# Kernel optimization log

Hardware: AMD Instinct MI355X
Metric: run time of the kernel (lower is better)

Reference implementation:

```python
import jax, jax.numpy as jnp
import numpy as np

DIM = 1024; HEADS = 8; DHEAD = 64; INNER = HEADS * DHEAD
WS = 512; B = 2; N = 2048; FF = 4 * DIM
NEG = -1e9


def layernorm(x, g, b, eps=1e-5):
    mu = jnp.mean(x, -1, keepdims=True)
    var = jnp.mean((x - mu) ** 2, -1, keepdims=True)
    return (x - mu) * jax.lax.rsqrt(var + eps) * g + b


def rmsnorm(x, g, eps=1e-6):
    return x * jax.lax.rsqrt(jnp.mean(x * x, -1, keepdims=True) + eps) * g


def rotate_half(x):
    x1, x2 = jnp.split(x, 2, -1)
    return jnp.concatenate([-x2, x1], -1)


def local_attention(q, k, v):
    # lucidrains LocalAttention: single-head over last dim, rotary pos emb,
    # window_size=WS, causal, look_backward=1, look_forward=0. n % WS == 0 so autopad no-op.
    b, n, d = q.shape
    w = n // WS
    inv_freq = 1.0 / (10000.0 ** (jnp.arange(0, d, 2, dtype=jnp.float32) / d))
    t = jnp.arange(n)
    freqs = t[:, None].astype(jnp.float32) * inv_freq[None, :]
    emb = jnp.concatenate([freqs, freqs], -1)           # [n, d]
    cos, sin = jnp.cos(emb), jnp.sin(emb)
    q = q * cos + rotate_half(q) * sin
    k = k * cos + rotate_half(k) * sin
    bq = q.reshape(b, w, WS, d) * (d ** -0.5)
    bk = k.reshape(b, w, WS, d)
    bv = v.reshape(b, w, WS, d)

    def look_around(x, pad_value):
        # gather current window + 1 window backward along the window axis
        pads = [(0, 0), (1, 0)] + [(0, 0)] * (x.ndim - 2)
        xp = jnp.pad(x, pads, constant_values=pad_value)
        return jnp.concatenate([xp[:, 0:w], xp[:, 1:w + 1]], axis=2)

    bk = look_around(bk, 0.0)                 # [b, w, 2*WS, d]
    bv = look_around(bv, 0.0)
    bt = t.reshape(w, WS)                     # query positions per window
    bqk = look_around(bt[None], -1)[0]        # key positions, pad = -1  [w, 2*WS]
    sim = jnp.einsum('bwie,bwje->bwij', bq, bk)  # [b, w, WS, 2*WS]
    mask = (bt[:, :, None] < bqk[:, None, :]) | (bqk[:, None, :] == -1)
    sim = jnp.where(mask[None], NEG, sim)
    attn = jax.nn.softmax(sim, -1)
    out = jnp.einsum('bwij,bwje->bwie', attn, bv)
    return out.reshape(b, n, d)


def setup_inputs() -> dict:
    key = jax.random.key(0)
    ks = jax.random.split(key, 10)
    s = 0.02
    f32 = jnp.float32
    return {
        'text': jax.random.normal(ks[0], (B, N, DIM), f32),
        'audio': jax.random.normal(ks[1], (B, N, DIM), f32),
        'video': jax.random.normal(ks[2], (B, N, DIM), f32),
        'Wa': jax.random.normal(ks[3], (DIM, DIM), f32) * s,
        'ba': jnp.zeros((DIM,), f32),
        'lna_g': jnp.ones((DIM,), f32), 'lna_b': jnp.zeros((DIM,), f32),
        'Wvid': jax.random.normal(ks[4], (DIM, DIM), f32) * s,
        'bvid': jnp.zeros((DIM,), f32),
        'lnv_g': jnp.ones((DIM,), f32), 'lnv_b': jnp.zeros((DIM,), f32),
        'ln1_g': jnp.ones((DIM,), f32), 'ln1_b': jnp.zeros((DIM,), f32),
        'Wq': jax.random.normal(ks[5], (DIM, INNER), f32) * s,
        'Wkv': jax.random.normal(ks[6], (DIM, 2 * INNER), f32) * s,
        'qn_g': jnp.ones((DHEAD,), f32), 'kn_g': jnp.ones((DHEAD,), f32),
        'Wo': jax.random.normal(ks[7], (INNER, DIM), f32) * s,
        'W1': jax.random.normal(ks[8], (DIM, FF), f32) * s,
        'b1': jnp.zeros((FF,), f32),
        'ln2_g': jnp.ones((FF,), f32), 'ln2_b': jnp.zeros((FF,), f32),
        'W2': jax.random.normal(ks[9], (FF, DIM), f32) * s,
        'b2': jnp.zeros((DIM,), f32),
    }


def reference(text, audio, video, Wa, ba, lna_g, lna_b, Wvid, bvid, lnv_g, lnv_b,
              ln1_g, ln1_b, Wq, Wkv, qn_g, kn_g, Wo, W1, b1, ln2_g, ln2_b, W2, b2):
    # modality -> text-token adapters (audio_to_text / video_to_text): linear + layernorm
    audio_t = layernorm(audio @ Wa + ba, lna_g, lna_b)
    video_t = layernorm(video @ Wvid + bvid, lnv_g, lnv_b)
    # windowed local attention: q=text, k=audio tokens, v=video tokens
    x = local_attention(text, audio_t, video_t)          # [B, N, DIM]
    # qk-norm full causal attention (flash=False: dense [B,H,N,N] scores)
    b, n, _ = x.shape
    h = layernorm(x, ln1_g, ln1_b)
    q = (h @ Wq).reshape(b, n, HEADS, DHEAD).transpose(0, 2, 1, 3)
    k, v = jnp.split(h @ Wkv, 2, -1)
    k = k.reshape(b, n, HEADS, DHEAD).transpose(0, 2, 1, 3)
    v = v.reshape(b, n, HEADS, DHEAD).transpose(0, 2, 1, 3)
    q = rmsnorm(q, qn_g)
    k = rmsnorm(k, kn_g)
    sim = jnp.einsum('bhid,bhjd->bhij', q, k) * (DHEAD ** -0.5)
    causal = jnp.tril(jnp.ones((n, n), bool))
    sim = jnp.where(causal[None, None], sim, NEG)
    attn = jax.nn.softmax(sim, -1)
    o = jnp.einsum('bhij,bhjd->bhid', attn, v).transpose(0, 2, 1, 3).reshape(b, n, INNER)
    x = o @ Wo
    x = x + x                                            # x = x + x in source
    # FFN: Linear -> GELU -> post-act LayerNorm -> Linear, + residual
    h1 = layernorm(jax.nn.gelu(x @ W1 + b1), ln2_g, ln2_b)
    return h1 @ W2 + b2 + x
```

## Files before the change

### kernel.cpp

```cpp
#include <hip/hip_runtime.h>
#include <hip/hip_bf16.h>

typedef __bf16 bf16;
typedef __bf16 bf16x8 __attribute__((ext_vector_type(8)));
typedef float  f32x4  __attribute__((ext_vector_type(4)));

static __device__ __forceinline__ float b2f(bf16 x) { return (float)x; }
static __device__ __forceinline__ bf16  f2b(float x) { return (bf16)x; }
static __device__ __forceinline__ float ldval(float v) { return v; }
static __device__ __forceinline__ float ldval(bf16 v)  { return (float)v; }

static __device__ __forceinline__ unsigned pk2(float a, float b)
{
    bf16 x = f2b(a), y = f2b(b);
    unsigned short ux = *(unsigned short*)&x;
    unsigned short uy = *(unsigned short*)&y;
    return (unsigned)ux | ((unsigned)uy << 16);
}

static __device__ __forceinline__ void gl_lds16(const bf16* g, bf16* l)
{
    __builtin_amdgcn_global_load_lds(
        (const __attribute__((address_space(1))) void*)g,
        (__attribute__((address_space(3))) void*)l,
        16, 0, 0);
}

__global__ void detect_dtype(const unsigned short* __restrict__ p, int* __restrict__ flag)
{
    if (threadIdx.x == 0 && blockIdx.x == 0) {
        int big = 0;
        for (int i = 0; i < 512; ++i) {
            int e = (p[i] >> 7) & 0xFF;
            if (e >= 0xE0) big++;
        }
        *flag = (big > 0) ? 1 : 0;
    }
}

__global__ __launch_bounds__(256) void convert2(
    const void* __restrict__ sa, const void* __restrict__ sb,
    bf16* __restrict__ da, bf16* __restrict__ db, int n,
    const int* __restrict__ flag)
{
    int f = *flag;
    int half = gridDim.x >> 1;
    const void* s = (blockIdx.x < half) ? sa : sb;
    bf16* d = (blockIdx.x < half) ? da : db;
    int bid = (blockIdx.x < half) ? blockIdx.x : blockIdx.x - half;
    for (int i = bid * 256 + threadIdx.x; i < n; i += half * 256) {
        float v = f ? ((const float*)s)[i] : (float)((const bf16*)s)[i];
        d[i] = f2b(v);
    }
}

struct VecPack { const void* src[14]; int n[14]; };
__global__ __launch_bounds__(256) void convert_vecs(
    VecPack vp, bf16* __restrict__ dst, const int* __restrict__ flag)
{
    int v = blockIdx.x;
    int f = *flag;
    const void* s = vp.src[v];
    int n = vp.n[v];
    bf16* d = dst + (size_t)v * 4096;
    for (int i = threadIdx.x; i < n; i += 256) {
        float x = f ? ((const float*)s)[i] : (float)((const bf16*)s)[i];
        d[i] = f2b(x);
    }
}

template <int EPI, int MT>
__global__ __launch_bounds__(256) void gemm_bt(
    const bf16* __restrict__ A0, int lda, int zsA, int zsA2,
    const bf16* __restrict__ B0, int ldb, int zsB, int zsB2,
    void* __restrict__ C0, int ldc, int zsC, int zsC2,
    const bf16* __restrict__ bias, int zsBias, float scale, int K)
{
    constexpr int IFR = MT / 32;
    __shared__ __align__(16) bf16 As[MT * 64];
    __shared__ __align__(16) bf16 Bs[128 * 64];
    const int z = blockIdx.z;
    const bf16* A  = A0 + (size_t)z * zsA + (size_t)(z >> 2) * zsA2;
    const bf16* Bt = B0 + (size_t)z * zsB + (size_t)(z >> 2) * zsB2;
    const size_t cbase = (size_t)z * zsC + (size_t)(z >> 2) * zsC2;
    if (bias) bias += (size_t)z * zsBias;
    const int tid  = threadIdx.x;
    const int lane = tid & 63, wave = tid >> 6;
    const int quad = lane >> 4, l16 = lane & 15;
    const size_t tm = (size_t)blockIdx.y * MT, tn = (size_t)blockIdx.x * 128;
    const int wm = (wave >> 1) * (MT / 2), wn = (wave & 1) * 64;
    const int srow = lane >> 3;
    const int scol = ((lane & 7) ^ srow) * 8;

    f32x4 acc[IFR][4];
    const f32x4 zro = {0.f, 0.f, 0.f, 0.f};
    #pragma unroll
    for (int i = 0; i < IFR; ++i)
        #pragma unroll
        for (int j = 0; j < 4; ++j) acc[i][j] = zro;

    const int swzA = l16 & 7;
    for (int k0 = 0; k0 < K; k0 += 64) {
        #pragma unroll
        for (int i = 0; i < IFR; ++i) {
            int chunk = (wave * IFR + i) * 64;
            int row = (chunk >> 3) + srow;
            gl_lds16(A + (tm + row) * (size_t)lda + k0 + scol, As + (size_t)chunk * 8);
        }
        #pragma unroll
        for (int i = 0; i < 4; ++i) {
            int chunk = (wave * 4 + i) * 64;
            int row = (chunk >> 3) + srow;
            gl_lds16(Bt + (tn + row) * (size_t)ldb + k0 + scol, Bs + (size_t)chunk * 8);
        }
        __syncthreads();
        #pragma unroll
        for (int kk = 0; kk < 2; ++kk) {
            bf16x8 af[IFR], bfr[4];
            #pragma unroll
            for (int i = 0; i < IFR; ++i) {
                int row = wm + i * 16 + l16;
                af[i] = *(const bf16x8*)(const void*)&As[(row * 8 + ((kk*4 + quad) ^ swzA)) * 8];
            }
            #pragma unroll
            for (int j = 0; j < 4; ++j) {
                int row = wn + j * 16 + l16;
                bfr[j] = *(const bf16x8*)(const void*)&Bs[(row * 8 + ((kk*4 + quad) ^ swzA)) * 8];
            }
            #pragma unroll
            for (int i = 0; i < IFR; ++i)
                #pragma unroll
                for (int j = 0; j < 4; ++j)
                    acc[i][j] = __builtin_amdgcn_mfma_f32_16x16x32_bf16(
                        af[i], bfr[j], acc[i][j], 0, 0, 0);
        }
        __syncthreads();
    }

    float* Cf = (float*)C0;
    bf16*  Cb = (bf16*)C0;
    #pragma unroll
    for (int i = 0; i < IFR; ++i) {
        #pragma unroll
        for (int j = 0; j < 4; ++j) {
            size_t col = tn + wn + j*16 + l16;
            float bb = bias ? b2f(bias[col]) : 0.f;
            #pragma unroll
            for (int r = 0; r < 4; ++r) {
                size_t row = tm + wm + i*16 + quad*4 + r;
                float v = acc[i][j][r] + bb;
                size_t off = cbase + row * (size_t)ldc + col;
                if (EPI == 0) {
                    Cf[off] = v;
                } else if (EPI == 1) {
                    Cb[off] = f2b(v * scale);
                } else {
                    float g = 0.5f * v * (1.f + tanhf(0.7978845608028654f *
                                  (v + 0.044715f * v * v * v)));
                    Cb[off] = f2b(g);
                }
            }
        }
    }
}

__global__ __launch_bounds__(512, 2) void gemm_ff1_8ph(
    const bf16* __restrict__ A, int lda,
    const bf16* __restrict__ Bt, int ldb,
    bf16* __restrict__ C, int ldc,
    const bf16* __restrict__ bias, int K)
{
    __shared__ __align__(16) bf16 As[2][256 * 64];
    __shared__ __align__(16) bf16 Bs[2][256 * 64];
    const int tid  = threadIdx.x;
    const int lane = tid & 63, wave = tid >> 6;
    const int quad = lane >> 4, l16 = lane & 15;
    const int wr = wave >> 2, wc = wave & 3;
    const size_t tm = (size_t)blockIdx.y * 256;
    const size_t tn = (size_t)blockIdx.x * 256;
    const int srow = lane >> 3;
    const int scol = ((lane & 7) ^ srow) * 8;
    const int swz  = l16 & 7;

    f32x4 acc[8][4];
    const f32x4 zro = {0.f, 0.f, 0.f, 0.f};
    #pragma unroll
    for (int m = 0; m < 8; ++m)
        #pragma unroll
        for (int n = 0; n < 4; ++n) acc[m][n] = zro;

    const bf16* aSrc[4];
    const bf16* bSrc[4];
    #pragma unroll
    for (int i = 0; i < 4; ++i) {
        int grow = wave * 32 + i * 8 + srow;
        aSrc[i] = A  + (tm + grow) * (size_t)lda + scol;
        bSrc[i] = Bt + (tn + grow) * (size_t)ldb + scol;
    }

#define STAGE(BUF, K0, I)                                                     \
    do {                                                                      \
        gl_lds16(aSrc[I] + (K0), &As[BUF][(wave * 4 + (I)) * 512]);           \
        gl_lds16(bSrc[I] + (K0), &Bs[BUF][(wave * 4 + (I)) * 512]);           \
    } while (0)

#define LDA_F(BUF, M, KK)                                                     \
    (*(const bf16x8*)(const void*)&As[BUF][(wr * 128 + (M) * 16 + l16) * 64 + \
        ((((KK) * 4 + quad) ^ swz) << 3)])
#define LDB_F(BUF, N, KK)                                                     \
    (*(const bf16x8*)(const void*)&Bs[BUF][(wc * 64 + (N) * 16 + l16) * 64 +  \
        ((((KK) * 4 + quad) ^ swz) << 3)])

#define PHASE(M0, M1, PREF_STMT, TAIL_STMT)                                   \
    {                                                                         \
        PREF_STMT;                                                            \
        bf16x8 x0 = LDA_F(cur, M0, 0), x1 = LDA_F(cur, M0, 1);                \
        bf16x8 y0 = LDA_F(cur, M1, 0), y1 = LDA_F(cur, M1, 1);                \
        asm volatile("s_barrier" ::: "memory");                               \
        __builtin_amdgcn_s_setprio(1);                                        \
        _Pragma("unroll")                                                     \
        for (int n = 0; n < 4; ++n) {                                         \
            acc[M0][n] = __builtin_amdgcn_mfma_f32_16x16x32_bf16(x0, bfr[n][0], acc[M0][n], 0, 0, 0); \
            acc[M0][n] = __builtin_amdgcn_mfma_f32_16x16x32_bf16(x1, bfr[n][1], acc[M0][n], 0, 0, 0); \
            acc[M1][n] = __builtin_amdgcn_mfma_f32_16x16x32_bf16(y0, bfr[n][0], acc[M1][n], 0, 0, 0); \
            acc[M1][n] = __builtin_amdgcn_mfma_f32_16x16x32_bf16(y1, bfr[n][1], acc[M1][n], 0, 0, 0); \
        }                                                                     \
        __builtin_amdgcn_s_setprio(0);                                        \
        TAIL_STMT;                                                            \
        asm volatile("s_barrier" ::: "memory");                               \
    }

    #pragma unroll
    for (int i = 0; i < 4; ++i) STAGE(0, 0, i);
    asm volatile("s_waitcnt vmcnt(0)" ::: "memory");
    asm volatile("s_barrier" ::: "memory");

    const int NT = K >> 6;
    bf16x8 bfr[4][2];
    for (int t = 0; t < NT; ++t) {
        const int cur = t & 1, nxt = cur ^ 1;
        const int k1  = (t + 1) << 6;
        const bool pref = (t + 1 < NT);

        #pragma unroll
        for (int n = 0; n < 4; ++n) {
            bfr[n][0] = LDB_F(cur, n, 0);
            bfr[n][1] = LDB_F(cur, n, 1);
        }
        PHASE(0, 1,
              if (pref) { STAGE(nxt, k1, 0); STAGE(nxt, k1, 1); }, )
        PHASE(2, 3,
              if (pref) { STAGE(nxt, k1, 2); STAGE(nxt, k1, 3); }, )
        PHASE(4, 5, , )
        PHASE(6, 7, ,
              asm volatile("s_waitcnt vmcnt(0)" ::: "memory"))
    }
#undef PHASE
#undef LDB_F
#undef LDA_F
#undef STAGE

    #pragma unroll
    for (int m = 0; m < 8; ++m) {
        #pragma unroll
        for (int n = 0; n < 4; ++n) {
            size_t col = tn + wc * 64 + n * 16 + l16;
            float bb = b2f(bias[col]);
            #pragma unroll
            for (int r = 0; r < 4; ++r) {
                size_t row = tm + wr * 128 + m * 16 + quad * 4 + r;
                float v = acc[m][n][r] + bb;
                float s = v * (1.5957691216057308f + 0.07135481627f * v * v);
                float g = v / (1.f + __expf(-s));
                C[row * (size_t)ldc + col] = f2b(g);
            }
        }
    }
}

__global__ void transpose_any(const void* __restrict__ in, int R, int C,
                              unsigned short* __restrict__ out, int ldo,
                              const int* __restrict__ flag)
{
    __shared__ unsigned short t[32][33];
    int f = *flag;
    int c0 = blockIdx.x * 32, r0 = blockIdx.y * 32;
    int tx = threadIdx.x, ty = threadIdx.y;
    for (int i = ty; i < 32; i += 8) {
        size_t idx = (size_t)(r0 + i) * C + c0 + tx;
        bf16 v = f ? f2b(((const float*)in)[idx]) : ((const bf16*)in)[idx];
        t[i][tx] = *(unsigned short*)&v;
    }
    __syncthreads();
    for (int i = ty; i < 32; i += 8)
        out[(size_t)(c0 + i) * ldo + r0 + tx] = t[tx][i];
}

__global__ void transpose_vt(const unsigned short* __restrict__ in,
                             unsigned short* __restrict__ out)
{
    __shared__ unsigned short t[32][33];
    int b = blockIdx.z;
    const unsigned short* src = in + (size_t)b * 2048 * 1024;
    unsigned short* dst = out + (size_t)b * 1024 * 2560;
    int c0 = blockIdx.x * 32, r0 = blockIdx.y * 32;
    int tx = threadIdx.x, ty = threadIdx.y;
    for (int i = ty; i < 32; i += 8)
        t[i][tx] = src[(size_t)(r0 + i) * 1024 + c0 + tx];
    __syncthreads();
    for (int i = ty; i < 32; i += 8)
        dst[(size_t)(c0 + i) * 2560 + 512 + r0 + tx] = t[tx][i];
}

__global__ void transpose_v(const float* __restrict__ qkv, bf16* __restrict__ Vt)
{
    __shared__ float t[32][33];
    int bh = blockIdx.z, b = bh >> 3, h = bh & 7;
    const float* src = qkv + (size_t)b * 2048 * 1536 + 1024 + h * 64;
    int c0 = blockIdx.x * 32, r0 = blockIdx.y * 32;
    int tx = threadIdx.x, ty = threadIdx.y;
    for (int i = ty; i < 32; i += 8)
        t[i][tx] = src[(size_t)(r0 + i) * 1536 + c0 + tx];
    __syncthreads();
    bf16* dst = Vt + (size_t)bh * 64 * 2048;
    for (int i = ty; i < 32; i += 8)
        dst[(size_t)(c0 + i) * 2048 + r0 + tx] = f2b(t[tx][i]);
}

template <typename Tin>
__global__ __launch_bounds__(256) void ln_rows(
    const Tin* __restrict__ in, int C,
    const bf16* __restrict__ g, const bf16* __restrict__ b,
    bf16* __restrict__ out, float eps)
{
    const int row = blockIdx.x, tid = threadIdx.x;
    const Tin* p = in + (size_t)row * C;
    float s = 0.f, ss = 0.f;
    for (int c = tid; c < C; c += 256) {
        float v = ldval(p[c]);
        s += v; ss += v * v;
    }
    #pragma unroll
    for (int d = 32; d > 0; d >>= 1) { s += __shfl_xor(s, d); ss += __shfl_xor(ss, d); }
    __shared__ float red[2][4];
    int wave = tid >> 6, lane = tid & 63;
    if (lane == 0) { red[0][wave] = s; red[1][wave] = ss; }
    __syncthreads();
    s  = red[0][0] + red[0][1] + red[0][2] + red[0][3];
    ss = red[1][0] + red[1][1] + red[1][2] + red[1][3];
    float mu   = s / C;
    float var  = ss / C - mu * mu;
    float rstd = rsqrtf(var + eps);
    bf16* q = out + (size_t)row * C;
    for (int c = tid; c < C; c += 256) {
        float v = ldval(p[c]);
        q[c] = f2b((v - mu) * rstd * b2f(g[c]) + b2f(b[c]));
    }
}

__global__ __launch_bounds__(256) void ln_rows2(
    const bf16* __restrict__ in,
    const bf16* __restrict__ g0, const bf16* __restrict__ b0,
    const bf16* __restrict__ g1, const bf16* __restrict__ b1,
    bf16* __restrict__ out0, bf16* __restrict__ out1)
{
    const int row = blockIdx.x, tid = threadIdx.x;
    const int sel = row >> 12;
    const bf16* p = in + (size_t)row * 1024;
    const bf16* g = sel ? g1 : g0;
    const bf16* b = sel ? b1 : b0;
    bf16* q = (sel ? out1 + (size_t)(row - 4096) * 1024 : out0 + (size_t)row * 1024);
    float s = 0.f, ss = 0.f;
    for (int c = tid; c < 1024; c += 256) {
        float v = b2f(p[c]);
        s += v; ss += v * v;
    }
    #pragma unroll
    for (int d = 32; d > 0; d >>= 1) { s += __shfl_xor(s, d); ss += __shfl_xor(ss, d); }
    __shared__ float red[2][4];
    int wave = tid >> 6, lane = tid & 63;
    if (lane == 0) { red[0][wave] = s; red[1][wave] = ss; }
    __syncthreads();
    s  = red[0][0] + red[0][1] + red[0][2] + red[0][3];
    ss = red[1][0] + red[1][1] + red[1][2] + red[1][3];
    float mu   = s * (1.f / 1024.f);
    float var  = ss * (1.f / 1024.f) - mu * mu;
    float rstd = rsqrtf(var + 1e-5f);
    for (int c = tid; c < 1024; c += 256) {
        float v = b2f(p[c]);
        q[c] = f2b((v - mu) * rstd * b2f(g[c]) + b2f(b[c]));
    }
}

__global__ __launch_bounds__(256) void rotary_kernel(
    const void* __restrict__ text, const int* __restrict__ flag,
    const bf16* __restrict__ audioT,
    bf16* __restrict__ qrot, bf16* __restrict__ krotPad)
{
    int row = blockIdx.x;
    int t = row & 2047, b = row >> 11;
    int tid = threadIdx.x;
    int f = *flag;
    const float lg = 9.210340371976184f / 512.f;
    size_t base = (size_t)row * 1024;
    size_t kb = ((size_t)(b * 2560 + 512 + t)) * 1024;
    for (int c = tid; c < 512; c += 256) {
        float invf = __expf(-(float)c * lg);
        float th = (float)t * invf;
        float sn, cs;
        sincosf(th, &sn, &cs);
        float q1 = f ? ((const float*)text)[base + c]
                     : b2f(((const bf16*)text)[base + c]);
        float q2 = f ? ((const float*)text)[base + c + 512]
                     : b2f(((const bf16*)text)[base + c + 512]);
        qrot[base + c]       = f2b((q1 * cs - q2 * sn) * 0.03125f);
        qrot[base + c + 512] = f2b((q2 * cs + q1 * sn) * 0.03125f);
        float k1 = b2f(audioT[base + c]), k2 = b2f(audioT[base + c + 512]);
        krotPad[kb + c]       = f2b(k1 * cs - k2 * sn);
        krotPad[kb + c + 512] = f2b(k2 * cs + k1 * sn);
    }
}

__global__ __launch_bounds__(256) void softmax_local(
    const float* __restrict__ sim, bf16* __restrict__ attn)
{
    int i  = blockIdx.x;
    int zz = blockIdx.y;
    int w  = zz & 3;
    int tid = threadIdx.x;
    const float* p = sim + ((size_t)zz * 512 + i) * 1024;
    bf16* q = attn + ((size_t)zz * 512 + i) * 1024;
    int jlo = (w == 0) ? 512 : 0;
    int jhi = 512 + i;
    float m = -1e30f;
    #pragma unroll
    for (int k = 0; k < 4; ++k) {
        int c = tid + k * 256;
        if (c >= jlo && c <= jhi) m = fmaxf(m, p[c]);
    }
    #pragma unroll
    for (int d = 32; d > 0; d >>= 1) m = fmaxf(m, __shfl_xor(m, d));
    __shared__ float red[2][4];
    int wave = tid >> 6, lane = tid & 63;
    if (lane == 0) red[0][wave] = m;
    __syncthreads();
    m = fmaxf(fmaxf(red[0][0], red[0][1]), fmaxf(red[0][2], red[0][3]));
    float pv[4];
    float s = 0.f;
    #pragma unroll
    for (int k = 0; k < 4; ++k) {
        int c = tid + k * 256;
        float e = (c >= jlo && c <= jhi) ? __expf(p[c] - m) : 0.f;
        pv[k] = e; s += e;
    }
    #pragma unroll
    for (int d = 32; d > 0; d >>= 1) s += __shfl_xor(s, d);
    if (lane == 0) red[1][wave] = s;
    __syncthreads();
    s = red[1][0] + red[1][1] + red[1][2] + red[1][3];
    float inv = 1.f / s;
    #pragma unroll
    for (int k = 0; k < 4; ++k) q[tid + k * 256] = f2b(pv[k] * inv);
}

__global__ __launch_bounds__(256) void pack_qk(
    const float* __restrict__ qkv, bf16* __restrict__ Qp, bf16* __restrict__ Kp,
    const bf16* __restrict__ qn_g, const bf16* __restrict__ kn_g)
{
    int gid  = blockIdx.x * 4 + (threadIdx.x >> 6);
    int lane = threadIdx.x & 63;
    int token = gid >> 4, r = gid & 15, part = r >> 3, h = r & 7;
    const float* p = qkv + (size_t)token * 1536 + part * 512 + h * 64 + lane;
    float v = *p;
    float ss = v * v;
    #pragma unroll
    for (int d = 32; d > 0; d >>= 1) ss += __shfl_xor(ss, d);
    float sc = rsqrtf(ss * (1.f / 64.f) + 1e-6f);
    const bf16* gw = part ? kn_g : qn_g;
    float outv = v * sc * b2f(gw[lane]);
    if (!part) outv *= 0.125f;
    int b = token >> 11, t = token & 2047;
    bf16* dst = (part ? Kp : Qp) + ((size_t)(b * 8 + h) * 2048 + t) * 64 + lane;
    *dst = f2b(outv);
}

__global__ __launch_bounds__(128) void flash_fused5(
    const bf16* __restrict__ Qp, const bf16* __restrict__ Kp,
    const bf16* __restrict__ Vt, bf16* __restrict__ o)
{
    __shared__ __align__(16) bf16 Ks[64][72];
    __shared__ __align__(16) bf16 Vs[64][72];
    __shared__ __align__(16) bf16 Ps[2][16][72];
    const int qb = 63 - blockIdx.x;
    const int bh = blockIdx.y, b = bh >> 3, h = bh & 7;
    const int qm = qb * 32;
    const int tid = threadIdx.x, wave = tid >> 6, lane = tid & 63;
    const int quad = lane >> 4, l16 = lane & 15;
    const bf16* Qg = Qp + (size_t)bh * 2048 * 64;
    const bf16* Kg = Kp + (size_t)bh * 2048 * 64;
    const bf16* Vg = Vt + (size_t)bh * 64 * 2048;

    const int q_row = qm + wave * 16 + l16;
    bf16x8 qa[2];
    qa[0] = *(const bf16x8*)(const void*)(Qg + (size_t)q_row * 64 + quad * 8);
    qa[1] = *(const bf16x8*)(const void*)(Qg + (size_t)q_row * 64 + 32 + quad * 8);

    f32x4 oacc[4];
    const f32x4 zro = {0.f, 0.f, 0.f, 0.f};
    #pragma unroll
    for (int j = 0; j < 4; ++j) oacc[j] = zro;
    float mst = -1e30f, lst = 0.f;

    const int ldr = tid >> 1, ldc = (tid & 1) * 32;
    const int nt = (qb >> 1) + 1;

    for (int t = 0; t < nt; ++t) {
        const int jt = t * 64;
        #pragma unroll
        for (int c = 0; c < 4; ++c) {
            *(uint4*)(void*)&Ks[ldr][ldc + c * 8] =
                *(const uint4*)(const void*)(Kg + (size_t)(jt + ldr) * 64 + ldc + c * 8);
            *(uint4*)(void*)&Vs[ldr][ldc + c * 8] =
                *(const uint4*)(const void*)(Vg + (size_t)ldr * 2048 + jt + ldc + c * 8);
        }
        __syncthreads();

        f32x4 s[4];
        #pragma unroll
        for (int j = 0; j < 4; ++j) s[j] = zro;
        #pragma unroll
        for (int kk = 0; kk < 2; ++kk) {
            #pragma unroll
            for (int j = 0; j < 4; ++j) {
                bf16x8 kf = *(const bf16x8*)(const void*)&Ks[j*16 + l16][kk*32 + quad*8];
                s[j] = __builtin_amdgcn_mfma_f32_16x16x32_bf16(kf, qa[kk], s[j], 0, 0, 0);
            }
        }

        if (jt + 63 > q_row) {
            #pragma unroll
            for (int j = 0; j < 4; ++j) {
                #pragma unroll
                for (int r = 0; r < 4; ++r) {
                    int key = jt + j * 16 + quad * 4 + r;
                    if (key > q_row) s[j][r] = -1e30f;
                }
            }
        }

        float mq = s[0][0];
        #pragma unroll
        for (int j = 0; j < 4; ++j)
            #pragma unroll
            for (int r = 0; r < 4; ++r) mq = fmaxf(mq, s[j][r]);
        float sq = 0.f;
        #pragma unroll
        for (int j = 0; j < 4; ++j)
            #pragma unroll
            for (int r = 0; r < 4; ++r) {
                float v = __expf(s[j][r] - mq);
                s[j][r] = v; sq += v;
            }

        float mo = __shfl_xor(mq, 16);
        float so = __shfl_xor(sq, 16);
        float mm = fmaxf(mq, mo);
        sq = sq * __expf(mq - mm) + so * __expf(mo - mm);
        float mo2 = __shfl_xor(mm, 32);
        float so2 = __shfl_xor(sq, 32);
        float mtile = fmaxf(mm, mo2);
        float stile = sq * __expf(mm - mtile) + so2 * __expf(mo2 - mtile);

        float mn  = fmaxf(mst, mtile);
        float scl = __expf(mst - mn);
        lst = lst * scl + stile * __expf(mtile - mn);
        mst = mn;
        float pf = __expf(mq - mn);

        float sclq[4];
        #pragma unroll
        for (int r = 0; r < 4; ++r) sclq[r] = __shfl(scl, quad * 4 + r);
        #pragma unroll
        for (int j = 0; j < 4; ++j)
            #pragma unroll
            for (int r = 0; r < 4; ++r) oacc[j][r] *= sclq[r];

        #pragma unroll
        for (int j = 0; j < 4; ++j) {
            uint2 u;
            u.x = pk2(s[j][0] * pf, s[j][1] * pf);
            u.y = pk2(s[j][2] * pf, s[j][3] * pf);
            *(uint2*)(void*)&Ps[wave][l16][j * 16 + quad * 4] = u;
        }
        bf16x8 pa0 = *(const bf16x8*)(const void*)&Ps[wave][l16][quad * 8];
        bf16x8 pa1 = *(const bf16x8*)(const void*)&Ps[wave][l16][32 + quad * 8];

        #pragma unroll
        for (int j = 0; j < 4; ++j) {
            bf16x8 vb = *(const bf16x8*)(const void*)&Vs[j*16 + l16][quad*8];
            oacc[j] = __builtin_amdgcn_mfma_f32_16x16x32_bf16(pa0, vb, oacc[j], 0, 0, 0);
        }
        #pragma unroll
        for (int j = 0; j < 4; ++j) {
            bf16x8 vb = *(const bf16x8*)(const void*)&Vs[j*16 + l16][32 + quad*8];
            oacc[j] = __builtin_amdgcn_mfma_f32_16x16x32_bf16(pa1, vb, oacc[j], 0, 0, 0);
        }
        __syncthreads();
    }

    float invq[4];
    #pragma unroll
    for (int r = 0; r < 4; ++r) invq[r] = 1.f / __shfl(lst, quad * 4 + r);
    #pragma unroll
    for (int j = 0; j < 4; ++j) {
        #pragma unroll
        for (int r = 0; r < 4; ++r) {
            int tr = qm + wave * 16 + quad * 4 + r;
            o[((size_t)(b * 2048 + tr)) * 512 + h * 64 + j * 16 + l16] =
                f2b(oacc[j][r] * invq[r]);
        }
    }
}

__global__ __launch_bounds__(256) void combine_ff2(
    const float* __restrict__ p0, const float* __restrict__ p1,
    const bf16* __restrict__ x2, const bf16* __restrict__ b2,
    float* __restrict__ out)
{
    int i4 = (blockIdx.x * 256 + threadIdx.x) * 4;
    #pragma unroll
    for (int k = 0; k < 4; ++k) {
        int i = i4 + k;
        out[i] = p0[i] + p1[i] + b2f(x2[i]) + b2f(b2[i & 1023]);
    }
}

static void launch_gemm(int epi, hipStream_t s,
                        const bf16* A, int lda, int zsA, int zsA2,
                        const bf16* Bt, int ldb, int zsB, int zsB2,
                        void* C, int ldc, int zsC, int zsC2,
                        const bf16* bias, int zsBias, float scale,
                        int M, int N, int K, int nz)
{
    bool mt64 = ((M >> 7) * (N >> 7) * nz) <= 512;
    dim3 blk(256);
    if (mt64) {
        dim3 g(N / 128, M / 64, nz);
        switch (epi) {
        case 0: gemm_bt<0,64><<<g, blk, 0, s>>>(A, lda, zsA, zsA2, Bt, ldb, zsB, zsB2, C, ldc, zsC, zsC2, bias, zsBias, scale, K); break;
        case 1: gemm_bt<1,64><<<g, blk, 0, s>>>(A, lda, zsA, zsA2, Bt, ldb, zsB, zsB2, C, ldc, zsC, zsC2, bias, zsBias, scale, K); break;
        default: gemm_bt<2,64><<<g, blk, 0, s>>>(A, lda, zsA, zsA2, Bt, ldb, zsB, zsB2, C, ldc, zsC, zsC2, bias, zsBias, scale, K); break;
        }
    } else {
        dim3 g(N / 128, M / 128, nz);
        switch (epi) {
        case 0: gemm_bt<0,128><<<g, blk, 0, s>>>(A, lda, zsA, zsA2, Bt, ldb, zsB, zsB2, C, ldc, zsC, zsC2, bias, zsBias, scale, K); break;
        case 1: gemm_bt<1,128><<<g, blk, 0, s>>>(A, lda, zsA, zsA2, Bt, ldb, zsB, zsB2, C, ldc, zsC, zsC2, bias, zsBias, scale, K); break;
        default: gemm_bt<2,128><<<g, blk, 0, s>>>(A, lda, zsA, zsA2, Bt, ldb, zsB, zsB2, C, ldc, zsC, zsC2, bias, zsBias, scale, K); break;
        }
    }
}

extern "C" void kernel_launch(void* const* d_in, const int* in_sizes, int n_in,
                              void* d_out, int out_size, void* d_ws, size_t ws_size,
                              hipStream_t stream)
{
    const void* text  = d_in[0];
    const void* audio = d_in[1];
    const void* video = d_in[2];
    const void* Wa    = d_in[3];
    const void* ba    = d_in[4];
    const void* lna_g = d_in[5];
    const void* lna_b = d_in[6];
    const void* Wvid  = d_in[7];
    const void* bvid  = d_in[8];
    const void* lnv_g = d_in[9];
    const void* lnv_b = d_in[10];
    const void* ln1_g = d_in[11];
    const void* ln1_b = d_in[12];
    const void* Wq    = d_in[13];
    const void* Wkv   = d_in[14];
    const void* qn_g  = d_in[15];
    const void* kn_g  = d_in[16];
    const void* Wo    = d_in[17];
    const void* W1    = d_in[18];
    const void* b1    = d_in[19];
    const void* ln2_g = d_in[20];
    const void* ln2_b = d_in[21];
    const void* W2    = d_in[22];
    const void* b2    = d_in[23];

    char* ws = (char*)d_ws;
    size_t off = 0;
    auto alloc = [&](size_t bytes) -> char* {
        char* p = ws + off;
        off += (bytes + 255) & ~(size_t)255;
        return p;
    };
    const size_t MB = 1024 * 1024;
    int*  flag  = (int*)alloc(256);
    bf16* vecs  = (bf16*)alloc(14 * 4096 * 2);
    bf16* WqkvT = (bf16*)alloc((size_t)1536 * 1024 * 2);
    bf16* WoT   = (bf16*)alloc((size_t)1024 * 512 * 2);
    bf16* W1T   = (bf16*)alloc((size_t)4096 * 1024 * 2);
    bf16* W2T   = (bf16*)alloc((size_t)1024 * 4096 * 2);
    char* regionIn = alloc(24 * MB);
    char* region2  = alloc(32 * MB);
    char* regionH  = alloc(8 * MB);
    char* regionX  = alloc(8 * MB);
    char* regionO  = alloc(4 * MB);
    bf16* qrot    = (bf16*)alloc((size_t)4096 * 1024 * 2);
    bf16* krotPad = (bf16*)alloc((size_t)2 * 2560 * 1024 * 2);
    bf16* VTpad   = (bf16*)alloc((size_t)2 * 1024 * 2560 * 2);
    bf16* attn    = (bf16*)alloc((size_t)8 * 512 * 1024 * 2);

    bf16*  audioC = (bf16*)regionIn;
    bf16*  videoC = audioC + (size_t)4096 * 1024;
    float* qkvF   = (float*)regionIn;
    bf16*  tmp2   = (bf16*)region2;
    float* tmpF   = (float*)region2;
    float* xF     = (float*)(region2 + 16 * MB);
    bf16*  g      = (bf16*)region2;
    bf16*  audioT = (bf16*)regionH;
    bf16*  h      = (bf16*)regionH;
    bf16*  videoT = (bf16*)regionX;
    bf16*  x2     = (bf16*)regionX;
    bf16*  WaT    = (bf16*)regionO;
    bf16*  WvT    = WaT + (size_t)1024 * 1024;
    bf16*  o      = (bf16*)regionO;
    bf16*  Qp     = qrot;
    bf16*  Kp     = krotPad;
    bf16*  Vth    = attn;
    float* p0     = (float*)regionIn;
    float* p1     = (float*)VTpad;

    bf16* baC   = vecs + 0 * 4096;
    bf16* bvidC = vecs + 1 * 4096;
    bf16* lnagC = vecs + 2 * 4096;
    bf16* lnabC = vecs + 3 * 4096;
    bf16* lnvgC = vecs + 4 * 4096;
    bf16* lnvbC = vecs + 5 * 4096;
    bf16* ln1gC = vecs + 6 * 4096;
    bf16* ln1bC = vecs + 7 * 4096;
    bf16* qngC  = vecs + 8 * 4096;
    bf16* kngC  = vecs + 9 * 4096;
    bf16* b1C   = vecs + 10 * 4096;
    bf16* ln2gC = vecs + 11 * 4096;
    bf16* ln2bC = vecs + 12 * 4096;
    bf16* b2C   = vecs + 13 * 4096;

    detect_dtype<<<1, 64, 0, stream>>>((const unsigned short*)text, flag);

    const int NTOK = 4096 * 1024;
    convert2<<<4096, 256, 0, stream>>>(audio, video, audioC, videoC, NTOK, flag);
    VecPack vp;
    const void* vsrc[14] = {ba, bvid, lna_g, lna_b, lnv_g, lnv_b, ln1_g, ln1_b,
                            qn_g, kn_g, b1, ln2_g, ln2_b, b2};
    int vn[14] = {1024, 1024, 1024, 1024, 1024, 1024, 1024, 1024,
                  64, 64, 4096, 4096, 4096, 1024};
    for (int i = 0; i < 14; ++i) { vp.src[i] = vsrc[i]; vp.n[i] = vn[i]; }
    convert_vecs<<<14, 256, 0, stream>>>(vp, vecs, flag);

    dim3 tb(32, 8);
    transpose_any<<<dim3(32, 32), tb, 0, stream>>>(Wa, 1024, 1024, (unsigned short*)WaT, 1024, flag);
    transpose_any<<<dim3(32, 32), tb, 0, stream>>>(Wvid, 1024, 1024, (unsigned short*)WvT, 1024, flag);
    transpose_any<<<dim3(16, 32), tb, 0, stream>>>(Wq, 1024, 512, (unsigned short*)WqkvT, 1024, flag);
    transpose_any<<<dim3(32, 32), tb, 0, stream>>>(Wkv, 1024, 1024, (unsigned short*)(WqkvT + (size_t)512 * 1024), 1024, flag);
    transpose_any<<<dim3(32, 16), tb, 0, stream>>>(Wo, 512, 1024, (unsigned short*)WoT, 512, flag);
    transpose_any<<<dim3(128, 32), tb, 0, stream>>>(W1, 1024, 4096, (unsigned short*)W1T, 1024, flag);
    transpose_any<<<dim3(32, 128), tb, 0, stream>>>(W2, 4096, 1024, (unsigned short*)W2T, 4096, flag);

    launch_gemm(1, stream, audioC, 1024, 4096*1024, 0, WaT, 1024, 1024*1024, 0,
                tmp2, 1024, 4096*1024, 0, baC, 4096, 1.f, 4096, 1024, 1024, 2);
    ln_rows2<<<8192, 256, 0, stream>>>(tmp2, lnagC, lnabC, lnvgC, lnvbC, audioT, videoT);

    hipMemsetAsync(krotPad, 0, (size_t)2 * 2560 * 1024 * 2, stream);
    hipMemsetAsync(VTpad, 0, (size_t)2 * 1024 * 2560 * 2, stream);
    rotary_kernel<<<4096, 256, 0, stream>>>(text, flag, audioT, qrot, krotPad);
    transpose_vt<<<dim3(32, 64, 2), tb, 0, stream>>>(
        (const unsigned short*)videoT, (unsigned short*)VTpad);

    launch_gemm(0, stream, qrot, 1024, 512*1024, 0,
                krotPad, 1024, 512*1024, 512*1024,
                tmpF, 1024, 512*1024, 0, nullptr, 0, 1.f, 512, 1024, 1024, 8);
    softmax_local<<<dim3(512, 8), 256, 0, stream>>>(tmpF, attn);
    launch_gemm(0, stream, attn, 1024, 512*1024, 0,
                VTpad, 2560, 512, 1024*2560 - 2048,
                xF, 1024, 512*1024, 0, nullptr, 0, 1.f, 512, 1024, 1024, 8);

    ln_rows<float><<<4096, 256, 0, stream>>>(xF, 1024, ln1gC, ln1bC, h, 1e-5f);
    launch_gemm(0, stream, h, 1024, 0, 0, WqkvT, 1024, 0, 0,
                qkvF, 1536, 0, 0, nullptr, 0, 1.f, 4096, 1536, 1024, 1);
    pack_qk<<<16384, 256, 0, stream>>>(qkvF, Qp, Kp, qngC, kngC);
    transpose_v<<<dim3(2, 64, 16), tb, 0, stream>>>(qkvF, Vth);
    flash_fused5<<<dim3(64, 16), 128, 0, stream>>>(Qp, Kp, Vth, o);

    launch_gemm(1, stream, o, 512, 0, 0, WoT, 512, 0, 0,
                x2, 1024, 0, 0, nullptr, 0, 2.f, 4096, 1024, 512, 1);
    gemm_ff1_8ph<<<dim3(16, 16), 512, 0, stream>>>(x2, 1024, W1T, 1024,
                                                   g, 4096, b1C, 1024);
    ln_rows<bf16><<<4096, 256, 0, stream>>>(g, 4096, ln2gC, ln2bC, g, 1e-5f);
    launch_gemm(0, stream, g, 4096, 2048, 0, W2T, 4096, 2048, 0,
                p0, 1024, (int)(p1 - p0), 0, nullptr, 0, 1.f, 4096, 1024, 2048, 2);
    combine_ff2<<<4096, 256, 0, stream>>>(p0, p1, x2, b2C, (float*)d_out);

    (void)in_sizes; (void)n_in; (void)out_size; (void)ws_size;
}
```

Baseline: 569.4 us.

## Split long causal flash-attention query blocks across two KV chunks with combine

The flash attention kernel now launches extra blocks so that the 32 longest causal query blocks per head split their KV range in half, each writing unnormalized partial outputs plus running max and sum to scratch. A new combine kernel merges the two partials with log-sum-exp rescaling and writes the bf16 output. This targets load imbalance and the tail, where a few blocks process up to 32 KV tiles while the short ones finish early. In exchange it adds fp32 partial traffic, a second kernel launch, and reuse of the regionIn scratch buffer.

```diff
diff --git a/kernel.cpp b/kernel.cpp
--- a/kernel.cpp
+++ b/kernel.cpp
@@ -484,14 +484,18 @@
     *dst = f2b(outv);
 }
 
-__global__ __launch_bounds__(128) void flash_fused5(
+__global__ __launch_bounds__(128) void flash_fused6(
     const bf16* __restrict__ Qp, const bf16* __restrict__ Kp,
-    const bf16* __restrict__ Vt, bf16* __restrict__ o)
+    const bf16* __restrict__ Vt, bf16* __restrict__ o,
+    float* __restrict__ Opart, float* __restrict__ MLpart)
 {
     __shared__ __align__(16) bf16 Ks[64][72];
     __shared__ __align__(16) bf16 Vs[64][72];
     __shared__ __align__(16) bf16 Ps[2][16][72];
-    const int qb = 63 - blockIdx.x;
+    const int bx = blockIdx.x;
+    const int qb = (bx < 64) ? (63 - bx) : (63 - (bx - 64));
+    const int chunk = (bx < 64) ? 0 : 1;
+    const bool split = (qb >= 32);
     const int bh = blockIdx.y, b = bh >> 3, h = bh & 7;
     const int qm = qb * 32;
     const int tid = threadIdx.x, wave = tid >> 6, lane = tid & 63;
@@ -500,6 +504,11 @@
     const bf16* Kg = Kp + (size_t)bh * 2048 * 64;
     const bf16* Vg = Vt + (size_t)bh * 64 * 2048;
 
+    const int nt_all = (qb >> 1) + 1;
+    const int half   = nt_all >> 1;
+    const int t0 = (split && chunk == 1) ? half : 0;
+    const int t1 = (split && chunk == 0) ? half : nt_all;
+
     const int q_row = qm + wave * 16 + l16;
     bf16x8 qa[2];
     qa[0] = *(const bf16x8*)(const void*)(Qg + (size_t)q_row * 64 + quad * 8);
@@ -512,9 +521,8 @@
     float mst = -1e30f, lst = 0.f;
 
     const int ldr = tid >> 1, ldc = (tid & 1) * 32;
-    const int nt = (qb >> 1) + 1;
-
-    for (int t = 0; t < nt; ++t) {
+
+    for (int t = t0; t < t1; ++t) {
         const int jt = t * 64;
         #pragma unroll
         for (int c = 0; c < 4; ++c) {
@@ -608,18 +616,59 @@
         __syncthreads();
     }
 
-    float invq[4];
-    #pragma unroll
-    for (int r = 0; r < 4; ++r) invq[r] = 1.f / __shfl(lst, quad * 4 + r);
-    #pragma unroll
-    for (int j = 0; j < 4; ++j) {
-        #pragma unroll
-        for (int r = 0; r < 4; ++r) {
-            int tr = qm + wave * 16 + quad * 4 + r;
-            o[((size_t)(b * 2048 + tr)) * 512 + h * 64 + j * 16 + l16] =
-                f2b(oacc[j][r] * invq[r]);
-        }
-    }
+    if (!split) {
+        float invq[4];
+        #pragma unroll
+        for (int r = 0; r < 4; ++r) invq[r] = 1.f / __shfl(lst, quad * 4 + r);
+        #pragma unroll
+        for (int j = 0; j < 4; ++j) {
+            #pragma unroll
+            for (int r = 0; r < 4; ++r) {
+                int tr = qm + wave * 16 + quad * 4 + r;
+                o[((size_t)(b * 2048 + tr)) * 512 + h * 64 + j * 16 + l16] =
+                    f2b(oacc[j][r] * invq[r]);
+            }
+        }
+    } else {
+        const int pidx = (bh * 32 + (qb - 32)) * 2 + chunk;
+        float* Od = Opart + (size_t)pidx * 2048;
+        #pragma unroll
+        for (int j = 0; j < 4; ++j)
+            #pragma unroll
+            for (int r = 0; r < 4; ++r) {
+                int lr = wave * 16 + quad * 4 + r;
+                Od[lr * 64 + j * 16 + l16] = oacc[j][r];
+            }
+        if (quad == 0) {
+            MLpart[(size_t)pidx * 64 + wave * 16 + l16]      = mst;
+            MLpart[(size_t)pidx * 64 + 32 + wave * 16 + l16] = lst;
+        }
+    }
+}
+
+__global__ __launch_bounds__(128) void flash_combine2(
+    const float* __restrict__ Opart, const float* __restrict__ MLpart,
+    bf16* __restrict__ o)
+{
+    int qb = 32 + blockIdx.x;
+    int bh = blockIdx.y, b = bh >> 3, h = bh & 7;
+    int base = (bh * 32 + (qb - 32)) * 2;
+    int row = threadIdx.x >> 2;
+    int d0  = (threadIdx.x & 3) * 16;
+    float m0 = MLpart[(size_t)base * 64 + row];
+    float l0 = MLpart[(size_t)base * 64 + 32 + row];
+    float m1 = MLpart[(size_t)(base + 1) * 64 + row];
+    float l1 = MLpart[(size_t)(base + 1) * 64 + 32 + row];
+    float mstar = fmaxf(m0, m1);
+    float w0 = __expf(m0 - mstar), w1 = __expf(m1 - mstar);
+    float inv = 1.f / (l0 * w0 + l1 * w1);
+    const float* O0 = Opart + (size_t)base * 2048 + row * 64 + d0;
+    const float* O1 = O0 + 2048;
+    int t = qb * 32 + row;
+    bf16* op = o + ((size_t)(b * 2048 + t)) * 512 + h * 64 + d0;
+    #pragma unroll 4
+    for (int dd = 0; dd < 16; ++dd)
+        op[dd] = f2b((O0[dd] * w0 + O1[dd] * w1) * inv);
 }
 
 __global__ __launch_bounds__(256) void combine_ff2(
@@ -731,6 +780,8 @@
     bf16*  Qp     = qrot;
     bf16*  Kp     = krotPad;
     bf16*  Vth    = attn;
+    float* Opart  = (float*)regionIn;
+    float* MLpart = Opart + (size_t)1024 * 2048;
     float* p0     = (float*)regionIn;
     float* p1     = (float*)VTpad;
 
@@ -793,7 +844,8 @@
                 qkvF, 1536, 0, 0, nullptr, 0, 1.f, 4096, 1536, 1024, 1);
     pack_qk<<<16384, 256, 0, stream>>>(qkvF, Qp, Kp, qngC, kngC);
     transpose_v<<<dim3(2, 64, 16), tb, 0, stream>>>(qkvF, Vth);
-    flash_fused5<<<dim3(64, 16), 128, 0, stream>>>(Qp, Kp, Vth, o);
+    flash_fused6<<<dim3(96, 16), 128, 0, stream>>>(Qp, Kp, Vth, o, Opart, MLpart);
+    flash_combine2<<<dim3(32, 16), 128, 0, stream>>>(Opart, MLpart, o);
 
     launch_gemm(1, stream, o, 512, 0, 0, WoT, 512, 0, 0,
                 x2, 1024, 0, 0, nullptr, 0, 2.f, 4096, 1024, 512, 1);
```

Result: no change. 565.7 us (-0.7%).
